# Kernel tuning notes

Hardware: AMD Instinct MI355X
Metric: run time of the kernel (lower is better)

The kernel has to match this reference:

```python
import jax, jax.numpy as jnp
import numpy as np

NOPE = 128          # qk_nope_head_dim
ROPE = 64           # qk_rope_head_dim
KV_LORA = 512       # kv_lora_rank
SCALE = (KV_LORA + ROPE) ** (-0.5)


def setup_inputs() -> dict:
    key = jax.random.key(0)
    k1, k2, k3, k4, k5 = jax.random.split(key, 5)
    T, H, K, S = 512, 128, 512, 8192
    q = jax.random.normal(k1, (T, H, NOPE + ROPE), dtype=jnp.float32)
    kv_cache = jax.random.normal(k2, (S, KV_LORA + ROPE), dtype=jnp.float32)
    topk_indices = jax.random.randint(k3, (T, K), 0, S, dtype=jnp.int32)
    k_b_proj_trans = jax.random.normal(k4, (H, KV_LORA, NOPE), dtype=jnp.float32) * 0.02
    v_b_proj = jax.random.normal(k5, (H, 128, KV_LORA), dtype=jnp.float32) * 0.02
    return {"q": q, "kv_cache": kv_cache, "topk_indices": topk_indices,
            "k_b_proj_trans": k_b_proj_trans, "v_b_proj": v_b_proj}


def reference(q, kv_cache, topk_indices, k_b_proj_trans, v_b_proj):
    # q: [T, H, 192]; kv_cache: [S, 576]; topk_indices: [T, K]
    q_nope, q_rope = q[..., :NOPE], q[..., NOPE:]
    # bmm_out(q_nope_t, k_b_proj_trans.transpose(1,2)): [T,H,128] x [H,512,128] -> [T,H,512]
    q_lat = jnp.einsum('thd,hkd->thk', q_nope, k_b_proj_trans)
    q_concat = jnp.concatenate([q_lat, q_rope], axis=-1)        # [T, H, 576]
    # sparse MLA: gather selected latent KV per token
    kv_sel = kv_cache[topk_indices]                              # [T, K, 576]
    scores = jnp.einsum('thc,tkc->thk', q_concat, kv_sel) * SCALE
    p = jax.nn.softmax(scores, axis=-1)                          # [T, H, K]
    attn_lat = jnp.einsum('thk,tkc->thc', p, kv_sel[..., :KV_LORA])  # [T, H, 512]
    # bmm_out(attn_lat_t, v_b_proj.transpose(1,2)): [T,H,512] x [H,512,128] -> [T,H,128]
    out = jnp.einsum('thc,hvc->thv', attn_lat, v_b_proj)
    return out
```

## Files before the change

### kernel.cpp

```cpp
#include <hip/hip_runtime.h>
#include <stdint.h>


#define SCALE 0.041666666666666664f

typedef __bf16 bf16x8 __attribute__((ext_vector_type(8)));
typedef float floatx4 __attribute__((ext_vector_type(4)));
typedef unsigned int uint32x2 __attribute__((ext_vector_type(2)));
typedef unsigned int uint32x4 __attribute__((ext_vector_type(4)));

static __device__ __forceinline__ unsigned short f2bf(float f) {
  unsigned int u = __builtin_bit_cast(unsigned int, f);
  u += 0x7FFF + ((u >> 16) & 1);
  return (unsigned short)(u >> 16);
}
static __device__ __forceinline__ float bf2f(unsigned short h) {
  unsigned int u = ((unsigned int)h) << 16;
  return __builtin_bit_cast(float, u);
}
static __device__ __forceinline__ unsigned int pack2(float lo, float hi) {
  return (unsigned int)f2bf(lo) | ((unsigned int)f2bf(hi) << 16);
}
static __device__ __forceinline__ void ldsdma16(const void* g, void* l) {
  __builtin_amdgcn_global_load_lds(
      (const __attribute__((address_space(1))) void*)g,
      (__attribute__((address_space(3))) void*)l, 16, 0, 0);
}
static __device__ __forceinline__ void issue_fence() {
  asm volatile("" ::: "memory");
  __builtin_amdgcn_sched_barrier(0);
}
static __device__ __forceinline__ unsigned int lds_addr(const void* p) {
  return (unsigned int)(unsigned long long)(
      (__attribute__((address_space(3))) const void*)p);
}
#define TR64(dst, addr, OFF) \
  asm volatile("ds_read_b64_tr_b16 %0, %1 offset:" OFF : "=v"(dst) : "v"(addr))

static __device__ __forceinline__ void stage8_f32(const float* __restrict__ src,
                                                  unsigned short* dst) {
  const float4* s4 = reinterpret_cast<const float4*>(src);
  float4 v0 = s4[0], v1 = s4[1];
  uint4 o;
  o.x = pack2(v0.x, v0.y); o.y = pack2(v0.z, v0.w);
  o.z = pack2(v1.x, v1.y); o.w = pack2(v1.z, v1.w);
  *reinterpret_cast<uint4*>(dst) = o;
}

static __device__ __forceinline__ void mfma_4x4(const unsigned short* As,
                                                const unsigned short* Bs,
                                                int wm, int wn, int l15, int quad,
                                                floatx4 acc[4][4]) {
  bf16x8 af[4], bfr[4];
#pragma unroll
  for (int i = 0; i < 4; ++i)
    af[i] = *reinterpret_cast<const bf16x8*>(&As[(wm + i * 16 + l15) * 32 + quad * 8]);
#pragma unroll
  for (int j = 0; j < 4; ++j)
    bfr[j] = *reinterpret_cast<const bf16x8*>(&Bs[(wn + j * 16 + l15) * 32 + quad * 8]);
#pragma unroll
  for (int i = 0; i < 4; ++i)
#pragma unroll
    for (int j = 0; j < 4; ++j)
      acc[i][j] = __builtin_amdgcn_mfma_f32_16x16x32_bf16(af[i], bfr[j], acc[i][j], 0, 0, 0);
}

__global__ void prep(const float* __restrict__ kv, unsigned short* __restrict__ kvb,
                     const float* __restrict__ q, unsigned short* __restrict__ qc) {
  int b = blockIdx.x;
  if (b < 4608) {
    int i = b * 256 + threadIdx.x;
    float4 v = reinterpret_cast<const float4*>(kv)[i];
    ushort4 o;
    o.x = f2bf(v.x); o.y = f2bf(v.y); o.z = f2bf(v.z); o.w = f2bf(v.w);
    reinterpret_cast<ushort4*>(kvb)[i] = o;
  } else {
    int i = (b - 4608) * 256 + threadIdx.x;
    int r = i & 63;
    int th = i >> 6;
    qc[(size_t)th * 576 + 512 + r] = f2bf(q[(size_t)th * 192 + 128 + r] * SCALE);
  }
}

__global__ __launch_bounds__(256) void qlat_gemm(const float* __restrict__ q,
                                                 const float* __restrict__ kb,
                                                 unsigned short* __restrict__ qc) {
  const int h = blockIdx.x;
  const int tm = (blockIdx.y & 3) * 128;
  const int tn = (blockIdx.y >> 2) * 128;
  __shared__ __align__(16) unsigned short As[128 * 32];
  __shared__ __align__(16) unsigned short Bs[128 * 32];
  const int tid = threadIdx.x;
  const int lane = tid & 63, wave = tid >> 6;
  const int wm = (wave & 1) * 64, wn = (wave >> 1) * 64;
  const int l15 = lane & 15, quad = lane >> 4;
  const int r0 = tid >> 2, cg = tid & 3;
  const float* a0 = q + ((size_t)(tm + r0) * 128 + h) * 192 + cg * 8;
  const float* a1 = q + ((size_t)(tm + r0 + 64) * 128 + h) * 192 + cg * 8;
  const float* b0 = kb + ((size_t)h * 512 + tn + r0) * 128 + cg * 8;
  const float* b1 = b0 + (size_t)64 * 128;
  floatx4 acc[4][4] = {};
  for (int ks = 0; ks < 4; ++ks) {
    stage8_f32(a0 + ks * 32, &As[tid * 8]);
    stage8_f32(a1 + ks * 32, &As[2048 + tid * 8]);
    stage8_f32(b0 + ks * 32, &Bs[tid * 8]);
    stage8_f32(b1 + ks * 32, &Bs[2048 + tid * 8]);
    __syncthreads();
    mfma_4x4(As, Bs, wm, wn, l15, quad, acc);
    __syncthreads();
  }
#pragma unroll
  for (int i = 0; i < 4; ++i) {
    const int row = wm + i * 16 + quad * 4;
#pragma unroll
    for (int j = 0; j < 4; ++j) {
      const int col = wn + j * 16 + l15;
#pragma unroll
      for (int r = 0; r < 4; ++r) {
        const int t = tm + row + r;
        qc[((size_t)t * 128 + h) * 576 + tn + col] = f2bf(acc[i][j][r] * SCALE);
      }
    }
  }
}

__global__ __launch_bounds__(256) void scores_gemm(const unsigned short* __restrict__ qc,
                                                   const unsigned short* __restrict__ kvb,
                                                   const int* __restrict__ topk,
                                                   unsigned short* __restrict__ P) {
  const int t = blockIdx.x;
  const int tn = blockIdx.y * 128;
  __shared__ __align__(16) unsigned short Bs[3][128 * 32];
  const int tid = threadIdx.x;
  const int lane = tid & 63, wave = tid >> 6;
  const int wm = (wave & 1) * 64, wn = (wave >> 1) * 64;
  const int l15 = lane & 15, quad = lane >> 4;
  const int r0 = tid >> 2, cg = tid & 3;
  const int idx0 = topk[t * 512 + tn + r0];
  const int idx1 = topk[t * 512 + tn + r0 + 64];
  const unsigned short* b0 = kvb + (size_t)idx0 * 576 + cg * 8;
  const unsigned short* b1 = kvb + (size_t)idx1 * 576 + cg * 8;
  const unsigned short* aab = qc + ((size_t)t * 128 + wm + l15) * 576 + quad * 8;
  floatx4 acc[4][4] = {};
  ldsdma16(b0, &Bs[0][tid * 8]);
  ldsdma16(b1, &Bs[0][2048 + tid * 8]);
  ldsdma16(b0 + 32, &Bs[1][tid * 8]);
  ldsdma16(b1 + 32, &Bs[1][2048 + tid * 8]);
  issue_fence();
  bf16x8 af[4], an[4];
#pragma unroll
  for (int i = 0; i < 4; ++i)
    af[i] = *reinterpret_cast<const bf16x8*>(aab + (size_t)i * 16 * 576);
  int bi = 0, bn = 2;
  for (int ks = 0; ks < 18; ++ks) {
    asm volatile("s_waitcnt vmcnt(6)" ::: "memory");
    __builtin_amdgcn_s_barrier();
    if (ks < 16) {
      ldsdma16(b0 + (ks + 2) * 32, &Bs[bn][tid * 8]);
      ldsdma16(b1 + (ks + 2) * 32, &Bs[bn][2048 + tid * 8]);
      issue_fence();
    }
    if (ks < 17) {
#pragma unroll
      for (int i = 0; i < 4; ++i)
        an[i] = *reinterpret_cast<const bf16x8*>(
            aab + (ks + 1) * 32 + (size_t)i * 16 * 576);
    }
    bf16x8 bfr[4];
#pragma unroll
    for (int j = 0; j < 4; ++j)
      bfr[j] = *reinterpret_cast<const bf16x8*>(
          &Bs[bi][(wn + j * 16 + l15) * 32 + quad * 8]);
#pragma unroll
    for (int i = 0; i < 4; ++i)
#pragma unroll
      for (int j = 0; j < 4; ++j)
        acc[i][j] =
            __builtin_amdgcn_mfma_f32_16x16x32_bf16(af[i], bfr[j], acc[i][j], 0, 0, 0);
    __builtin_amdgcn_s_barrier();
#pragma unroll
    for (int i = 0; i < 4; ++i) af[i] = an[i];
    bi = bi == 2 ? 0 : bi + 1;
    bn = bn == 2 ? 0 : bn + 1;
  }
#pragma unroll
  for (int i = 0; i < 4; ++i) {
    const int row = wm + i * 16 + quad * 4;
#pragma unroll
    for (int j = 0; j < 4; ++j) {
      const int col = tn + wn + j * 16 + l15;
#pragma unroll
      for (int r = 0; r < 4; ++r)
        P[((size_t)t * 128 + row + r) * 512 + col] = f2bf(acc[i][j][r]);
    }
  }
}

__global__ __launch_bounds__(256) void softmax_rows(const unsigned short* __restrict__ Pin,
                                                    unsigned short* __restrict__ P2) {
  const int row = blockIdx.x * 4 + (threadIdx.x >> 6);
  const int t = row >> 7, h = row & 127;
  const int lane = threadIdx.x & 63;
  const unsigned short* rp = Pin + (size_t)row * 512 + lane * 8;
  uint4 raw = *reinterpret_cast<const uint4*>(rp);
  unsigned int w[4] = {raw.x, raw.y, raw.z, raw.w};
  float f[8];
  float mx = -1e30f;
#pragma unroll
  for (int i = 0; i < 8; ++i) {
    f[i] = bf2f((unsigned short)((w[i >> 1] >> ((i & 1) * 16)) & 0xFFFF));
    mx = fmaxf(mx, f[i]);
  }
#pragma unroll
  for (int off = 32; off; off >>= 1) mx = fmaxf(mx, __shfl_xor(mx, off, 64));
  float s = 0.f;
#pragma unroll
  for (int i = 0; i < 8; ++i) { f[i] = __expf(f[i] - mx); s += f[i]; }
#pragma unroll
  for (int off = 32; off; off >>= 1) s += __shfl_xor(s, off, 64);
  const float inv = 1.0f / s;
  uint4 o;
  o.x = pack2(f[0] * inv, f[1] * inv);
  o.y = pack2(f[2] * inv, f[3] * inv);
  o.z = pack2(f[4] * inv, f[5] * inv);
  o.w = pack2(f[6] * inv, f[7] * inv);
  unsigned short* wp =
      P2 + (((size_t)t * 16 + (lane >> 2)) * 128 + h) * 32 + (lane & 3) * 8;
  *reinterpret_cast<uint4*>(wp) = o;
}

__global__ __launch_bounds__(512) void attn_gemm(const unsigned short* __restrict__ P2,
                                                 const unsigned short* __restrict__ kvb,
                                                 const int* __restrict__ topk,
                                                 unsigned short* __restrict__ alat) {
  const int t = blockIdx.x;
  __shared__ __align__(16) unsigned short St[3][32 * 512];
  const int tid = threadIdx.x;
  const int lane = tid & 63, wave = tid >> 6;
  const int wm = (wave >> 2) * 64;
  const int wc = wave & 3;
  const int l15 = lane & 15, quad = lane >> 4;
  const int keyBase = (tid >> 8) * 4 + ((tid >> 1) & 3);
  const int cA = ((tid >> 3) & 31) * 16 + (tid & 1) * 8;
  const int* tkrow = topk + t * 512;
  const unsigned short* a_base =
      P2 + ((size_t)t * 16 * 128 + wm + l15) * 32 + quad * 8;
  const unsigned int tra0 = lds_addr(&St[0][0]) + quad * 8192 + wc * 1024 + l15 * 8;
  floatx4 acc[4][8] = {};
  bf16x8 a_cur[4], a_nxt[4];
  int ip0, ip1, ip2, ip3;
  {
#pragma unroll
    for (int d = 0; d < 4; ++d) {
      const int k0 = tkrow[d * 8 + keyBase];
      ldsdma16(kvb + (size_t)k0 * 576 + cA, &St[0][d * 4096 + tid * 8]);
    }
#pragma unroll
    for (int i = 0; i < 4; ++i)
      a_cur[i] = *reinterpret_cast<const bf16x8*>(a_base + (size_t)i * 16 * 32);
    ip0 = tkrow[64 + 0 * 8 + keyBase];
    ip1 = tkrow[64 + 1 * 8 + keyBase];
    ip2 = tkrow[64 + 2 * 8 + keyBase];
    ip3 = tkrow[64 + 3 * 8 + keyBase];
    issue_fence();
#pragma unroll
    for (int d = 0; d < 4; ++d) {
      const int k1 = tkrow[32 + d * 8 + keyBase];
      ldsdma16(kvb + (size_t)k1 * 576 + cA, &St[1][d * 4096 + tid * 8]);
    }
  }
  int sti = 0, stp = 2;
  for (int ks = 0; ks < 16; ++ks) {
    asm volatile("s_waitcnt vmcnt(4)" ::: "memory");
    __builtin_amdgcn_s_barrier();
    const unsigned int tra = tra0 + sti * 32768;
    uint32x2 rl0, rl1, rl2, rl3, rl4, rl5, rl6, rl7;
    uint32x2 rh0, rh1, rh2, rh3, rh4, rh5, rh6, rh7;
    TR64(rl0, tra, "0");    TR64(rh0, tra, "4096");
    TR64(rl1, tra, "128");  TR64(rh1, tra, "4224");
    TR64(rl2, tra, "256");  TR64(rh2, tra, "4352");
    TR64(rl3, tra, "384");  TR64(rh3, tra, "4480");
    TR64(rl4, tra, "512");  TR64(rh4, tra, "4608");
    TR64(rl5, tra, "640");  TR64(rh5, tra, "4736");
    TR64(rl6, tra, "768");  TR64(rh6, tra, "4864");
    TR64(rl7, tra, "896");  TR64(rh7, tra, "4992");
    if (ks < 15) {
#pragma unroll
      for (int i = 0; i < 4; ++i)
        a_nxt[i] = *reinterpret_cast<const bf16x8*>(
            a_base + ((size_t)(ks + 1) * 128 + i * 16) * 32);
    }
    if (ks < 14) {
      const int d0 = ip0, d1 = ip1, d2 = ip2, d3 = ip3;
      if (ks < 13) {
        ip0 = tkrow[(ks + 3) * 32 + 0 * 8 + keyBase];
        ip1 = tkrow[(ks + 3) * 32 + 1 * 8 + keyBase];
        ip2 = tkrow[(ks + 3) * 32 + 2 * 8 + keyBase];
        ip3 = tkrow[(ks + 3) * 32 + 3 * 8 + keyBase];
      }
      issue_fence();
      ldsdma16(kvb + (size_t)d0 * 576 + cA, &St[stp][0 * 4096 + tid * 8]);
      ldsdma16(kvb + (size_t)d1 * 576 + cA, &St[stp][1 * 4096 + tid * 8]);
      ldsdma16(kvb + (size_t)d2 * 576 + cA, &St[stp][2 * 4096 + tid * 8]);
      ldsdma16(kvb + (size_t)d3 * 576 + cA, &St[stp][3 * 4096 + tid * 8]);
    }
    asm volatile("s_waitcnt lgkmcnt(0)");
    __builtin_amdgcn_sched_barrier(0);
    bf16x8 bfr[8];
    {
      uint32x4 w;
      w.x = rl0.x; w.y = rl0.y; w.z = rh0.x; w.w = rh0.y; bfr[0] = __builtin_bit_cast(bf16x8, w);
      w.x = rl1.x; w.y = rl1.y; w.z = rh1.x; w.w = rh1.y; bfr[1] = __builtin_bit_cast(bf16x8, w);
      w.x = rl2.x; w.y = rl2.y; w.z = rh2.x; w.w = rh2.y; bfr[2] = __builtin_bit_cast(bf16x8, w);
      w.x = rl3.x; w.y = rl3.y; w.z = rh3.x; w.w = rh3.y; bfr[3] = __builtin_bit_cast(bf16x8, w);
      w.x = rl4.x; w.y = rl4.y; w.z = rh4.x; w.w = rh4.y; bfr[4] = __builtin_bit_cast(bf16x8, w);
      w.x = rl5.x; w.y = rl5.y; w.z = rh5.x; w.w = rh5.y; bfr[5] = __builtin_bit_cast(bf16x8, w);
      w.x = rl6.x; w.y = rl6.y; w.z = rh6.x; w.w = rh6.y; bfr[6] = __builtin_bit_cast(bf16x8, w);
      w.x = rl7.x; w.y = rl7.y; w.z = rh7.x; w.w = rh7.y; bfr[7] = __builtin_bit_cast(bf16x8, w);
    }
#pragma unroll
    for (int i = 0; i < 4; ++i)
#pragma unroll
      for (int j = 0; j < 8; ++j)
        acc[i][j] =
            __builtin_amdgcn_mfma_f32_16x16x32_bf16(a_cur[i], bfr[j], acc[i][j], 0, 0, 0);
#pragma unroll
    for (int i = 0; i < 4; ++i) a_cur[i] = a_nxt[i];
    sti = sti == 2 ? 0 : sti + 1;
    stp = stp == 2 ? 0 : stp + 1;
  }
#pragma unroll
  for (int i = 0; i < 4; ++i) {
    const int row = wm + i * 16 + quad * 4;
#pragma unroll
    for (int j = 0; j < 8; ++j) {
      const int col = wc * 128 + j * 16 + l15;
#pragma unroll
      for (int r = 0; r < 4; ++r)
        alat[((size_t)(row + r) * 512 + t) * 512 + col] = f2bf(acc[i][j][r]);
    }
  }
}

__global__ __launch_bounds__(256) void out_gemm(const unsigned short* __restrict__ alat,
                                                const float* __restrict__ vb,
                                                float* __restrict__ out) {
  const int h = blockIdx.x;
  const int tm = blockIdx.y * 128;
  __shared__ __align__(16) unsigned short Bs[128 * 32];
  const int tid = threadIdx.x;
  const int lane = tid & 63, wave = tid >> 6;
  const int wm = (wave & 1) * 64, wn = (wave >> 1) * 64;
  const int l15 = lane & 15, quad = lane >> 4;
  const int r0 = tid >> 2, cg = tid & 3;
  const unsigned short* aab =
      alat + ((size_t)h * 512 + tm + wm + l15) * 512 + quad * 8;
  const float* b0 = vb + ((size_t)h * 128 + r0) * 512 + cg * 8;
  const float* b1 = b0 + (size_t)64 * 512;
  floatx4 acc[4][4] = {};
  for (int ks = 0; ks < 16; ++ks) {
    stage8_f32(b0 + ks * 32, &Bs[tid * 8]);
    stage8_f32(b1 + ks * 32, &Bs[2048 + tid * 8]);
    __syncthreads();
    bf16x8 af[4], bfr[4];
#pragma unroll
    for (int i = 0; i < 4; ++i)
      af[i] = *reinterpret_cast<const bf16x8*>(
          aab + ks * 32 + (size_t)i * 16 * 512);
#pragma unroll
    for (int j = 0; j < 4; ++j)
      bfr[j] = *reinterpret_cast<const bf16x8*>(
          &Bs[(wn + j * 16 + l15) * 32 + quad * 8]);
#pragma unroll
    for (int i = 0; i < 4; ++i)
#pragma unroll
      for (int j = 0; j < 4; ++j)
        acc[i][j] =
            __builtin_amdgcn_mfma_f32_16x16x32_bf16(af[i], bfr[j], acc[i][j], 0, 0, 0);
    __syncthreads();
  }
#pragma unroll
  for (int i = 0; i < 4; ++i) {
    const int row = wm + i * 16 + quad * 4;
#pragma unroll
    for (int j = 0; j < 4; ++j) {
      const int col = wn + j * 16 + l15;
#pragma unroll
      for (int r = 0; r < 4; ++r) {
        const int t = tm + row + r;
        out[((size_t)t * 128 + h) * 128 + col] = acc[i][j][r];
      }
    }
  }
}

extern "C" void kernel_launch(void* const* d_in, const int* in_sizes, int n_in,
                              void* d_out, int out_size, void* d_ws, size_t ws_size,
                              hipStream_t stream) {
  const float* q = (const float*)d_in[0];
  const float* kv = (const float*)d_in[1];
  const int* topk = (const int*)d_in[2];
  const float* kb = (const float*)d_in[3];
  const float* vb = (const float*)d_in[4];
  float* out = (float*)d_out;

  char* ws = (char*)d_ws;
  unsigned short* kvb = (unsigned short*)ws;
  unsigned short* qc = (unsigned short*)(ws + 9437184);
  unsigned short* P = (unsigned short*)(ws + 9437184 + 75497472);
  unsigned short* P2 = qc;
  unsigned short* alat = P;

  prep<<<dim3(20992), dim3(256), 0, stream>>>(kv, kvb, q, qc);
  qlat_gemm<<<dim3(128, 16), dim3(256), 0, stream>>>(q, kb, qc);
  scores_gemm<<<dim3(512, 4), dim3(256), 0, stream>>>(qc, kvb, topk, P);
  softmax_rows<<<dim3(16384), dim3(256), 0, stream>>>(P, P2);
  attn_gemm<<<dim3(512), dim3(512), 0, stream>>>(P2, kvb, topk, alat);
  out_gemm<<<dim3(128, 4), dim3(256), 0, stream>>>(alat, vb, out);
}
```

Baseline: 402.2 us.

## Store q_concat and attn latent in k-slab tiled layout for contiguous GEMM loads

```diff
diff --git a/kernel.cpp b/kernel.cpp
--- a/kernel.cpp
+++ b/kernel.cpp
@@ -66,7 +66,7 @@
 }
 
 __global__ void prep(const float* __restrict__ kv, unsigned short* __restrict__ kvb,
-                     const float* __restrict__ q, unsigned short* __restrict__ qc) {
+                     const float* __restrict__ q, unsigned short* __restrict__ qc2) {
   int b = blockIdx.x;
   if (b < 4608) {
     int i = b * 256 + threadIdx.x;
@@ -78,13 +78,15 @@
     int i = (b - 4608) * 256 + threadIdx.x;
     int r = i & 63;
     int th = i >> 6;
-    qc[(size_t)th * 576 + 512 + r] = f2bf(q[(size_t)th * 192 + 128 + r] * SCALE);
+    int t = th >> 7, h = th & 127;
+    qc2[(((size_t)t * 18 + 16 + (r >> 5)) * 128 + h) * 32 + (r & 31)] =
+        f2bf(q[(size_t)th * 192 + 128 + r] * SCALE);
   }
 }
 
 __global__ __launch_bounds__(256) void qlat_gemm(const float* __restrict__ q,
                                                  const float* __restrict__ kb,
-                                                 unsigned short* __restrict__ qc) {
+                                                 unsigned short* __restrict__ qc2) {
   const int h = blockIdx.x;
   const int tm = (blockIdx.y & 3) * 128;
   const int tn = (blockIdx.y >> 2) * 128;
@@ -114,17 +116,18 @@
     const int row = wm + i * 16 + quad * 4;
 #pragma unroll
     for (int j = 0; j < 4; ++j) {
-      const int col = wn + j * 16 + l15;
+      const int c = tn + wn + j * 16 + l15;
+      const int ks2 = c >> 5, kk = c & 31;
 #pragma unroll
       for (int r = 0; r < 4; ++r) {
         const int t = tm + row + r;
-        qc[((size_t)t * 128 + h) * 576 + tn + col] = f2bf(acc[i][j][r] * SCALE);
+        qc2[(((size_t)t * 18 + ks2) * 128 + h) * 32 + kk] = f2bf(acc[i][j][r] * SCALE);
       }
     }
   }
 }
 
-__global__ __launch_bounds__(256) void scores_gemm(const unsigned short* __restrict__ qc,
+__global__ __launch_bounds__(256) void scores_gemm(const unsigned short* __restrict__ qc2,
                                                    const unsigned short* __restrict__ kvb,
                                                    const int* __restrict__ topk,
                                                    unsigned short* __restrict__ P) {
@@ -140,7 +143,8 @@
   const int idx1 = topk[t * 512 + tn + r0 + 64];
   const unsigned short* b0 = kvb + (size_t)idx0 * 576 + cg * 8;
   const unsigned short* b1 = kvb + (size_t)idx1 * 576 + cg * 8;
-  const unsigned short* aab = qc + ((size_t)t * 128 + wm + l15) * 576 + quad * 8;
+  const unsigned short* aab =
+      qc2 + ((size_t)t * 2304 + wm + l15) * 32 + quad * 8;
   floatx4 acc[4][4] = {};
   ldsdma16(b0, &Bs[0][tid * 8]);
   ldsdma16(b1, &Bs[0][2048 + tid * 8]);
@@ -150,7 +154,7 @@
   bf16x8 af[4], an[4];
 #pragma unroll
   for (int i = 0; i < 4; ++i)
-    af[i] = *reinterpret_cast<const bf16x8*>(aab + (size_t)i * 16 * 576);
+    af[i] = *reinterpret_cast<const bf16x8*>(aab + i * 512);
   int bi = 0, bn = 2;
   for (int ks = 0; ks < 18; ++ks) {
     asm volatile("s_waitcnt vmcnt(6)" ::: "memory");
@@ -164,7 +168,7 @@
 #pragma unroll
       for (int i = 0; i < 4; ++i)
         an[i] = *reinterpret_cast<const bf16x8*>(
-            aab + (ks + 1) * 32 + (size_t)i * 16 * 576);
+            aab + (size_t)(ks + 1) * 4096 + i * 512);
     }
     bf16x8 bfr[4];
 #pragma unroll
@@ -232,7 +236,7 @@
 __global__ __launch_bounds__(512) void attn_gemm(const unsigned short* __restrict__ P2,
                                                  const unsigned short* __restrict__ kvb,
                                                  const int* __restrict__ topk,
-                                                 unsigned short* __restrict__ alat) {
+                                                 unsigned short* __restrict__ alat2) {
   const int t = blockIdx.x;
   __shared__ __align__(16) unsigned short St[3][32 * 512];
   const int tid = threadIdx.x;
@@ -334,15 +338,17 @@
     const int row = wm + i * 16 + quad * 4;
 #pragma unroll
     for (int j = 0; j < 8; ++j) {
-      const int col = wc * 128 + j * 16 + l15;
+      const int c = wc * 128 + j * 16 + l15;
+      const int ks2 = c >> 5, kk = c & 31;
 #pragma unroll
       for (int r = 0; r < 4; ++r)
-        alat[((size_t)(row + r) * 512 + t) * 512 + col] = f2bf(acc[i][j][r]);
-    }
-  }
-}
-
-__global__ __launch_bounds__(256) void out_gemm(const unsigned short* __restrict__ alat,
+        alat2[(((size_t)(row + r) * 16 + ks2) * 512 + t) * 32 + kk] =
+            f2bf(acc[i][j][r]);
+    }
+  }
+}
+
+__global__ __launch_bounds__(256) void out_gemm(const unsigned short* __restrict__ alat2,
                                                 const float* __restrict__ vb,
                                                 float* __restrict__ out) {
   const int h = blockIdx.x;
@@ -354,7 +360,7 @@
   const int l15 = lane & 15, quad = lane >> 4;
   const int r0 = tid >> 2, cg = tid & 3;
   const unsigned short* aab =
-      alat + ((size_t)h * 512 + tm + wm + l15) * 512 + quad * 8;
+      alat2 + ((size_t)h * 8192 + tm + wm + l15) * 32 + quad * 8;
   const float* b0 = vb + ((size_t)h * 128 + r0) * 512 + cg * 8;
   const float* b1 = b0 + (size_t)64 * 512;
   floatx4 acc[4][4] = {};
@@ -366,7 +372,7 @@
 #pragma unroll
     for (int i = 0; i < 4; ++i)
       af[i] = *reinterpret_cast<const bf16x8*>(
-          aab + ks * 32 + (size_t)i * 16 * 512);
+          aab + (size_t)ks * 16384 + i * 512);
 #pragma unroll
     for (int j = 0; j < 4; ++j)
       bfr[j] = *reinterpret_cast<const bf16x8*>(
@@ -406,15 +412,15 @@
 
   char* ws = (char*)d_ws;
   unsigned short* kvb = (unsigned short*)ws;
-  unsigned short* qc = (unsigned short*)(ws + 9437184);
+  unsigned short* qc2 = (unsigned short*)(ws + 9437184);
   unsigned short* P = (unsigned short*)(ws + 9437184 + 75497472);
-  unsigned short* P2 = qc;
-  unsigned short* alat = P;
-
-  prep<<<dim3(20992), dim3(256), 0, stream>>>(kv, kvb, q, qc);
-  qlat_gemm<<<dim3(128, 16), dim3(256), 0, stream>>>(q, kb, qc);
-  scores_gemm<<<dim3(512, 4), dim3(256), 0, stream>>>(qc, kvb, topk, P);
+  unsigned short* P2 = qc2;
+  unsigned short* alat2 = P;
+
+  prep<<<dim3(20992), dim3(256), 0, stream>>>(kv, kvb, q, qc2);
+  qlat_gemm<<<dim3(128, 16), dim3(256), 0, stream>>>(q, kb, qc2);
+  scores_gemm<<<dim3(512, 4), dim3(256), 0, stream>>>(qc2, kvb, topk, P);
   softmax_rows<<<dim3(16384), dim3(256), 0, stream>>>(P, P2);
-  attn_gemm<<<dim3(512), dim3(512), 0, stream>>>(P2, kvb, topk, alat);
-  out_gemm<<<dim3(128, 4), dim3(256), 0, stream>>>(alat, vb, out);
-}
+  attn_gemm<<<dim3(512), dim3(512), 0, stream>>>(P2, kvb, topk, alat2);
+  out_gemm<<<dim3(128, 4), dim3(256), 0, stream>>>(alat2, vb, out);
+}
```

New measurement: 384.6 us. 4.4% less time.
